# Kernel tuning notes

Measured on AMD Instinct MI355X. Metric: run time of the kernel, lower is better.

The kernel has to match this reference:

```python
import jax, jax.numpy as jnp
import numpy as np

TOP_K = 8
NUM_EXPERTS = 64
HIDDEN = 4096
ALPHA = 0.01


def setup_inputs() -> dict:
    key = jax.random.key(0)
    k1, k2 = jax.random.split(key)
    hidden_states = jax.random.normal(k1, (4, 4096, HIDDEN), dtype=jnp.float32)
    expert_gate_weights = jax.random.normal(k2, (NUM_EXPERTS, HIDDEN), dtype=jnp.float32) * 0.02
    return {"hidden_states": hidden_states, "expert_gate_weights": expert_gate_weights}


def reference(hidden_states, expert_gate_weights):
    # flatten tokens: [B,S,H] -> [T,H]
    flat_tokens = hidden_states.reshape(-1, HIDDEN)
    # router logits: F.linear(x, W) == x @ W.T -> [T,E]
    logits = jnp.einsum('th,eh->te', flat_tokens, expert_gate_weights)
    scores = jax.nn.softmax(logits, axis=-1)
    # top-k gating (lax.top_k returns sorted descending; torch used sorted=False
    # so only the ordering within the k slots may differ, not the set/values)
    topk_gates, local_indices = jax.lax.top_k(scores, TOP_K)  # [T,k], [T,k]
    topk_gates = topk_gates / (topk_gates.sum(axis=-1, keepdims=True) + 1e-6)
    # aux load-balance loss: one-hot counts (non-diff) * mean importance
    expert_counts = jnp.zeros((NUM_EXPERTS,), dtype=jnp.float32).at[local_indices.reshape(-1)].add(1.0)
    expert_importance = scores.mean(axis=0)  # [E]
    aux_loss = (expert_importance * expert_counts).sum() * ALPHA
    return local_indices, topk_gates, aux_loss
```

## Files before the change

### kernel.cpp

```cpp
#include <hip/hip_runtime.h>
#include <cstdint>
#include <cstddef>

#define NUM_TOK 16384
#define HID     4096
#define NEXP    64
#define TOPK    8

__global__ __launch_bounds__(256) void transpose_w(const float* __restrict__ W,
                                                   float* __restrict__ Wt) {
    int id4 = blockIdx.x * 256 + threadIdx.x;
    int e   = id4 >> 10;
    int k   = (id4 & 1023) << 2;
    float4 w = reinterpret_cast<const float4*>(W)[id4];
    Wt[(size_t)(k + 0) * NEXP + e] = w.x;
    Wt[(size_t)(k + 1) * NEXP + e] = w.y;
    Wt[(size_t)(k + 2) * NEXP + e] = w.z;
    Wt[(size_t)(k + 3) * NEXP + e] = w.w;
}

__device__ __forceinline__ float wave_sum(float v) {
#pragma unroll
    for (int off = 32; off >= 1; off >>= 1)
        v += __shfl_xor(v, off, 64);
    return v;
}

__global__ __launch_bounds__(512, 2) void router_fused(
    const float* __restrict__ hidden,
    const float* __restrict__ Wt,
    float* __restrict__ out_idx, float* __restrict__ out_gates,
    float* __restrict__ gImp, float* __restrict__ gCnt) {
    __shared__ float LDSp[4][64][65];

    const int tid  = threadIdx.x;
    const int lane = tid & 63;
    const int wave = __builtin_amdgcn_readfirstlane(tid >> 6);
    const int s    = wave & 3;
    const int h    = wave >> 2;
    const int lr   = lane >> 3;
    const int lc   = lane & 7;
    const int T0   = blockIdx.x * 64;
    const int t0   = h * 32 + lr * 4;
    const int e0   = lc * 8;

    const float* xb0 = hidden + (size_t)(T0 + t0 + 0) * HID + s * 1024;
    const float* xb1 = hidden + (size_t)(T0 + t0 + 1) * HID + s * 1024;
    const float* xb2 = hidden + (size_t)(T0 + t0 + 2) * HID + s * 1024;
    const float* xb3 = hidden + (size_t)(T0 + t0 + 3) * HID + s * 1024;
    const float* wb  = Wt + (size_t)(s * 1024) * NEXP + e0;

    float sl[4][8];
#pragma unroll
    for (int i = 0; i < 4; ++i)
#pragma unroll
        for (int j = 0; j < 8; ++j) sl[i][j] = 0.0f;

    for (int c = 0; c < 16; ++c) {
        const int xoff = c * 64;
        const float* wc = wb + (size_t)c * 64 * NEXP;

        float part[4][8];
#pragma unroll
        for (int i = 0; i < 4; ++i)
#pragma unroll
            for (int j = 0; j < 8; ++j) part[i][j] = 0.0f;

#pragma unroll
        for (int k4 = 0; k4 < 16; ++k4) {
            float4 xv0 = *reinterpret_cast<const float4*>(xb0 + xoff + k4 * 4);
            float4 xv1 = *reinterpret_cast<const float4*>(xb1 + xoff + k4 * 4);
            float4 xv2 = *reinterpret_cast<const float4*>(xb2 + xoff + k4 * 4);
            float4 xv3 = *reinterpret_cast<const float4*>(xb3 + xoff + k4 * 4);
            float xa[4][4] = {{xv0.x, xv0.y, xv0.z, xv0.w},
                              {xv1.x, xv1.y, xv1.z, xv1.w},
                              {xv2.x, xv2.y, xv2.z, xv2.w},
                              {xv3.x, xv3.y, xv3.z, xv3.w}};
#pragma unroll
            for (int j2 = 0; j2 < 4; ++j2) {
                float4 wA = *reinterpret_cast<const float4*>(wc + (size_t)(k4 * 4 + j2) * NEXP);
                float4 wB = *reinterpret_cast<const float4*>(wc + (size_t)(k4 * 4 + j2) * NEXP + 4);
                float wv[8] = {wA.x, wA.y, wA.z, wA.w, wB.x, wB.y, wB.z, wB.w};
#pragma unroll
                for (int i = 0; i < 4; ++i) {
                    float x = xa[i][j2];
#pragma unroll
                    for (int j = 0; j < 8; ++j)
                        part[i][j] = fmaf(x, wv[j], part[i][j]);
                }
            }
        }
#pragma unroll
        for (int i = 0; i < 4; ++i)
#pragma unroll
            for (int j = 0; j < 8; ++j) sl[i][j] += part[i][j];
    }

#pragma unroll
    for (int i = 0; i < 4; ++i)
#pragma unroll
        for (int j = 0; j < 8; ++j)
            LDSp[s][t0 + i][e0 + j] = sl[i][j];
    __syncthreads();

    if (wave == 0) {
        const int t = lane;
        float sc[NEXP];
#pragma unroll
        for (int e = 0; e < NEXP; ++e) {
            float v = LDSp[0][t][e];
            v += LDSp[1][t][e];
            v += LDSp[2][t][e];
            v += LDSp[3][t][e];
            sc[e] = v;
        }

        float m = sc[0];
#pragma unroll
        for (int e = 1; e < NEXP; ++e) m = fmaxf(m, sc[e]);
        float sum = 0.0f;
#pragma unroll
        for (int e = 0; e < NEXP; ++e) { sc[e] = expf(sc[e] - m); sum += sc[e]; }
#pragma unroll
        for (int e = 0; e < NEXP; ++e) sc[e] = sc[e] / sum;

        unsigned long long used = 0ull;
        float g[TOPK];
        float fid[TOPK];
#pragma unroll
        for (int r = 0; r < TOPK; ++r) {
            float best = -1.0f;
            int   bi   = 0;
#pragma unroll
            for (int e = 0; e < NEXP; ++e) {
                bool ok = (((used >> e) & 1ull) == 0ull) && (sc[e] > best);
                best = ok ? sc[e] : best;
                bi   = ok ? e : bi;
            }
            used |= (1ull << bi);
            g[r]   = best;
            fid[r] = (float)bi;
        }
        float gsum = ((g[0] + g[1]) + (g[2] + g[3])) +
                     ((g[4] + g[5]) + (g[6] + g[7])) + 1e-6f;
        float inv = 1.0f / gsum;

        int tg = T0 + t;
        float4 i0 = make_float4(fid[0], fid[1], fid[2], fid[3]);
        float4 i1 = make_float4(fid[4], fid[5], fid[6], fid[7]);
        float4 g0 = make_float4(g[0] * inv, g[1] * inv, g[2] * inv, g[3] * inv);
        float4 g1 = make_float4(g[4] * inv, g[5] * inv, g[6] * inv, g[7] * inv);
        *reinterpret_cast<float4*>(out_idx   + (size_t)tg * 8)     = i0;
        *reinterpret_cast<float4*>(out_idx   + (size_t)tg * 8 + 4) = i1;
        *reinterpret_cast<float4*>(out_gates + (size_t)tg * 8)     = g0;
        *reinterpret_cast<float4*>(out_gates + (size_t)tg * 8 + 4) = g1;

        float myImp = 0.0f, myCnt = 0.0f;
#pragma unroll
        for (int e = 0; e < NEXP; ++e) {
            float se = wave_sum(sc[e]);
            unsigned long long b = __ballot(((used >> e) & 1ull) != 0ull);
            if (lane == e) { myImp = se; myCnt = (float)__popcll(b); }
        }
        atomicAdd(&gImp[lane], myImp);
        atomicAdd(&gCnt[lane], myCnt);
    }
}

__global__ __launch_bounds__(64) void aux_kernel(const float* __restrict__ gImp,
                                                 const float* __restrict__ gCnt,
                                                 float* __restrict__ out_aux) {
    int lane = threadIdx.x;
    float v = gImp[lane] * gCnt[lane];
    v = wave_sum(v);
    if (lane == 0)
        *out_aux = v * (0.01f / (float)NUM_TOK);
}

extern "C" void kernel_launch(void* const* d_in, const int* in_sizes, int n_in,
                              void* d_out, int out_size, void* d_ws, size_t ws_size,
                              hipStream_t stream) {
    const float* hidden = (const float*)d_in[0];
    const float* W      = (const float*)d_in[1];

    float* out       = (float*)d_out;
    float* out_idx   = out;
    float* out_gates = out + (size_t)NUM_TOK * TOPK;
    float* out_aux   = out + (size_t)2 * NUM_TOK * TOPK;

    float* Wt   = (float*)d_ws;
    float* gImp = (float*)((char*)d_ws + (1 << 20));
    float* gCnt = gImp + NEXP;

    hipMemsetAsync(gImp, 0, 2 * NEXP * sizeof(float), stream);
    transpose_w<<<256, 256, 0, stream>>>(W, Wt);
    router_fused<<<NUM_TOK / 64, 512, 0, stream>>>(hidden, Wt, out_idx, out_gates,
                                                   gImp, gCnt);
    aux_kernel<<<1, 64, 0, stream>>>(gImp, gCnt, out_aux);
}
```

Before: 578.4 us.

## Stage hidden and weight tiles into LDS with double-buffered async global loads

Restructures the router GEMM so each block of 256 threads handles 32 tokens. Each 64-wide k-chunk of the hidden rows and transposed weights is copied into double-buffered LDS with global_load_lds, so the load of the next chunk overlaps the FMAs on the current one. This replaces per-thread direct global float4 loads and the cross-wave split-K reduction through LDS. The softmax/top-k then runs on 32 lanes per block instead of 64. The cost is a barrier per chunk, more blocks that each reload the full weight matrix, and a lower FMA count per thread for each loaded value.

```diff
diff --git a/kernel.cpp b/kernel.cpp
--- a/kernel.cpp
+++ b/kernel.cpp
@@ -6,6 +6,11 @@
 #define HID     4096
 #define NEXP    64
 #define TOPK    8
+#define TB      32
+#define XPAD    68
+
+typedef const float __attribute__((address_space(1)))* gptr_t;
+typedef float __attribute__((address_space(3)))* lptr_t;
 
 __global__ __launch_bounds__(256) void transpose_w(const float* __restrict__ W,
                                                    float* __restrict__ Wt) {
@@ -26,93 +31,111 @@
     return v;
 }
 
-__global__ __launch_bounds__(512, 2) void router_fused(
+__global__ __launch_bounds__(256, 2) void router_fused(
     const float* __restrict__ hidden,
     const float* __restrict__ Wt,
     float* __restrict__ out_idx, float* __restrict__ out_gates,
     float* __restrict__ gImp, float* __restrict__ gCnt) {
-    __shared__ float LDSp[4][64][65];
+    __shared__ __align__(16) float Xs[2][TB * XPAD];
+    __shared__ __align__(16) float Wsh[2][64 * NEXP];
 
     const int tid  = threadIdx.x;
     const int lane = tid & 63;
     const int wave = __builtin_amdgcn_readfirstlane(tid >> 6);
-    const int s    = wave & 3;
-    const int h    = wave >> 2;
     const int lr   = lane >> 3;
     const int lc   = lane & 7;
-    const int T0   = blockIdx.x * 64;
-    const int t0   = h * 32 + lr * 4;
+    const int row  = wave * 8 + lr;
     const int e0   = lc * 8;
-
-    const float* xb0 = hidden + (size_t)(T0 + t0 + 0) * HID + s * 1024;
-    const float* xb1 = hidden + (size_t)(T0 + t0 + 1) * HID + s * 1024;
-    const float* xb2 = hidden + (size_t)(T0 + t0 + 2) * HID + s * 1024;
-    const float* xb3 = hidden + (size_t)(T0 + t0 + 3) * HID + s * 1024;
-    const float* wb  = Wt + (size_t)(s * 1024) * NEXP + e0;
-
-    float sl[4][8];
-#pragma unroll
-    for (int i = 0; i < 4; ++i)
-#pragma unroll
-        for (int j = 0; j < 8; ++j) sl[i][j] = 0.0f;
-
-    for (int c = 0; c < 16; ++c) {
-        const int xoff = c * 64;
-        const float* wc = wb + (size_t)c * 64 * NEXP;
-
-        float part[4][8];
-#pragma unroll
-        for (int i = 0; i < 4; ++i)
-#pragma unroll
-            for (int j = 0; j < 8; ++j) part[i][j] = 0.0f;
+    const int T0   = blockIdx.x * TB;
+
+    auto stage = [&](int c) {
+        int buf = c & 1;
+#pragma unroll
+        for (int j = 0; j < 8; ++j) {
+            int r = wave * 8 + j;
+            const float* src = hidden + (size_t)(T0 + r) * HID + c * 64 + lane;
+            __builtin_amdgcn_global_load_lds((gptr_t)src,
+                                             (lptr_t)(&Xs[buf][r * XPAD + lane]), 4, 0, 0);
+        }
+#pragma unroll
+        for (int j = 0; j < 4; ++j) {
+            int i = wave * 4 + j;
+            const float* src = Wt + (size_t)c * (64 * NEXP) + i * 256 + lane * 4;
+            __builtin_amdgcn_global_load_lds((gptr_t)src,
+                                             (lptr_t)(&Wsh[buf][i * 256 + lane * 4]), 16, 0, 0);
+        }
+    };
+
+    float part[8], sliceSum[8], total[8];
+#pragma unroll
+    for (int j = 0; j < 8; ++j) { sliceSum[j] = 0.0f; total[j] = 0.0f; }
+
+    stage(0);
+    for (int c = 0; c < 64; ++c) {
+        __syncthreads();
+        if (c + 1 < 64) stage(c + 1);
+        const float* __restrict__ xrow = &Xs[c & 1][row * XPAD];
+        const float* __restrict__ wb   = &Wsh[c & 1][0];
+
+#pragma unroll
+        for (int j = 0; j < 8; ++j) part[j] = 0.0f;
 
 #pragma unroll
         for (int k4 = 0; k4 < 16; ++k4) {
-            float4 xv0 = *reinterpret_cast<const float4*>(xb0 + xoff + k4 * 4);
-            float4 xv1 = *reinterpret_cast<const float4*>(xb1 + xoff + k4 * 4);
-            float4 xv2 = *reinterpret_cast<const float4*>(xb2 + xoff + k4 * 4);
-            float4 xv3 = *reinterpret_cast<const float4*>(xb3 + xoff + k4 * 4);
-            float xa[4][4] = {{xv0.x, xv0.y, xv0.z, xv0.w},
-                              {xv1.x, xv1.y, xv1.z, xv1.w},
-                              {xv2.x, xv2.y, xv2.z, xv2.w},
-                              {xv3.x, xv3.y, xv3.z, xv3.w}};
+            float4 x4 = *reinterpret_cast<const float4*>(xrow + k4 * 4);
+            float xa[4] = {x4.x, x4.y, x4.z, x4.w};
 #pragma unroll
             for (int j2 = 0; j2 < 4; ++j2) {
-                float4 wA = *reinterpret_cast<const float4*>(wc + (size_t)(k4 * 4 + j2) * NEXP);
-                float4 wB = *reinterpret_cast<const float4*>(wc + (size_t)(k4 * 4 + j2) * NEXP + 4);
-                float wv[8] = {wA.x, wA.y, wA.z, wA.w, wB.x, wB.y, wB.z, wB.w};
-#pragma unroll
-                for (int i = 0; i < 4; ++i) {
-                    float x = xa[i][j2];
-#pragma unroll
-                    for (int j = 0; j < 8; ++j)
-                        part[i][j] = fmaf(x, wv[j], part[i][j]);
-                }
+                float4 wA = *reinterpret_cast<const float4*>(wb + (k4 * 4 + j2) * NEXP + e0);
+                float4 wB = *reinterpret_cast<const float4*>(wb + (k4 * 4 + j2) * NEXP + e0 + 4);
+                float x = xa[j2];
+                part[0] = fmaf(x, wA.x, part[0]);
+                part[1] = fmaf(x, wA.y, part[1]);
+                part[2] = fmaf(x, wA.z, part[2]);
+                part[3] = fmaf(x, wA.w, part[3]);
+                part[4] = fmaf(x, wB.x, part[4]);
+                part[5] = fmaf(x, wB.y, part[5]);
+                part[6] = fmaf(x, wB.z, part[6]);
+                part[7] = fmaf(x, wB.w, part[7]);
             }
         }
 #pragma unroll
-        for (int i = 0; i < 4; ++i)
-#pragma unroll
-            for (int j = 0; j < 8; ++j) sl[i][j] += part[i][j];
+        for (int j = 0; j < 8; ++j) sliceSum[j] += part[j];
+
+        if ((c & 15) == 15) {
+            if (c < 16) {
+#pragma unroll
+                for (int j = 0; j < 8; ++j) total[j] = sliceSum[j];
+            } else {
+#pragma unroll
+                for (int j = 0; j < 8; ++j) total[j] += sliceSum[j];
+            }
+#pragma unroll
+            for (int j = 0; j < 8; ++j) sliceSum[j] = 0.0f;
+        }
     }
 
-#pragma unroll
-    for (int i = 0; i < 4; ++i)
-#pragma unroll
-        for (int j = 0; j < 8; ++j)
-            LDSp[s][t0 + i][e0 + j] = sl[i][j];
+    float* Ep = &Xs[0][0];
+    *reinterpret_cast<float4*>(Ep + row * XPAD + e0) =
+        make_float4(total[0], total[1], total[2], total[3]);
+    *reinterpret_cast<float4*>(Ep + row * XPAD + e0 + 4) =
+        make_float4(total[4], total[5], total[6], total[7]);
     __syncthreads();
 
-    if (wave == 0) {
-        const int t = lane;
-        float sc[NEXP];
-#pragma unroll
-        for (int e = 0; e < NEXP; ++e) {
-            float v = LDSp[0][t][e];
-            v += LDSp[1][t][e];
-            v += LDSp[2][t][e];
-            v += LDSp[3][t][e];
-            sc[e] = v;
+    float sc[NEXP];
+#pragma unroll
+    for (int e = 0; e < NEXP; ++e) sc[e] = 0.0f;
+    unsigned long long used = 0ull;
+
+    if (tid < TB) {
+        const float* srow = Ep + tid * XPAD;
+#pragma unroll
+        for (int e4 = 0; e4 < NEXP / 4; ++e4) {
+            float4 v = *reinterpret_cast<const float4*>(srow + e4 * 4);
+            sc[e4 * 4 + 0] = v.x;
+            sc[e4 * 4 + 1] = v.y;
+            sc[e4 * 4 + 2] = v.z;
+            sc[e4 * 4 + 3] = v.w;
         }
 
         float m = sc[0];
@@ -124,7 +147,6 @@
 #pragma unroll
         for (int e = 0; e < NEXP; ++e) sc[e] = sc[e] / sum;
 
-        unsigned long long used = 0ull;
         float g[TOPK];
         float fid[TOPK];
 #pragma unroll
@@ -145,16 +167,18 @@
                      ((g[4] + g[5]) + (g[6] + g[7])) + 1e-6f;
         float inv = 1.0f / gsum;
 
-        int tg = T0 + t;
+        int t = T0 + tid;
         float4 i0 = make_float4(fid[0], fid[1], fid[2], fid[3]);
         float4 i1 = make_float4(fid[4], fid[5], fid[6], fid[7]);
         float4 g0 = make_float4(g[0] * inv, g[1] * inv, g[2] * inv, g[3] * inv);
         float4 g1 = make_float4(g[4] * inv, g[5] * inv, g[6] * inv, g[7] * inv);
-        *reinterpret_cast<float4*>(out_idx   + (size_t)tg * 8)     = i0;
-        *reinterpret_cast<float4*>(out_idx   + (size_t)tg * 8 + 4) = i1;
-        *reinterpret_cast<float4*>(out_gates + (size_t)tg * 8)     = g0;
-        *reinterpret_cast<float4*>(out_gates + (size_t)tg * 8 + 4) = g1;
-
+        *reinterpret_cast<float4*>(out_idx   + (size_t)t * 8)     = i0;
+        *reinterpret_cast<float4*>(out_idx   + (size_t)t * 8 + 4) = i1;
+        *reinterpret_cast<float4*>(out_gates + (size_t)t * 8)     = g0;
+        *reinterpret_cast<float4*>(out_gates + (size_t)t * 8 + 4) = g1;
+    }
+
+    if (wave == 0) {
         float myImp = 0.0f, myCnt = 0.0f;
 #pragma unroll
         for (int e = 0; e < NEXP; ++e) {
@@ -194,7 +218,7 @@
 
     hipMemsetAsync(gImp, 0, 2 * NEXP * sizeof(float), stream);
     transpose_w<<<256, 256, 0, stream>>>(W, Wt);
-    router_fused<<<NUM_TOK / 64, 512, 0, stream>>>(hidden, Wt, out_idx, out_gates,
+    router_fused<<<NUM_TOK / TB, 256, 0, stream>>>(hidden, Wt, out_idx, out_gates,
                                                    gImp, gCnt);
     aux_kernel<<<1, 64, 0, stream>>>(gImp, gCnt, out_aux);
 }
```

Result: faster. 497.7 us (-14.0%).
